# Performance work log

Hardware: AMD Instinct MI355X
Metric: run time of the kernel (lower is better)

Reference implementation:

```python
import jax, jax.numpy as jnp
import numpy as np

B, NMAX, D, NUM = 1024, 128, 256, 4
EPS = 1e-8
NEG = -1e9


def segment_softmax(logits, seg):
    # torch_geometric-style softmax over ragged segments. logits: (T,)
    m = jax.ops.segment_max(logits, seg, num_segments=B)
    e = jnp.exp(logits - m[seg])
    s = jax.ops.segment_sum(e, seg, num_segments=B)
    return e / (s[seg] + 1e-16)


def to_dense(v, seg, pos):
    # scatter ragged rows into (B, NMAX, ...) dense batch
    return jnp.zeros((B, NMAX) + v.shape[1:], v.dtype).at[seg, pos].set(v)


def uot_badmm(x, q0d, maskf, a1, a2, a3, rho):
    # Bregman-ADMM solver for entropic unbalanced OT (f_method='badmm-e').
    # x: (B,N,D) cost (to be maximized); q0d, maskf: (B,N,1); a1,a2,a3,rho: (NUM,)
    log_p0 = jnp.full((B, 1, D), -jnp.log(float(D)), x.dtype)  # uniform dim prior
    log_q0 = jnp.log(q0d + EPS)                                # (B,N,1)
    log_t = log_q0 + log_p0                                    # T init = q0 p0^T
    log_s = log_t
    log_mu = log_p0
    log_eta = log_q0
    z = jnp.zeros_like(x)
    z1 = jnp.zeros_like(log_p0)
    z2 = jnp.zeros_like(log_q0)
    neg = (1.0 - maskf) * NEG  # exclude padded rows from N-axis softmax
    for k in range(NUM):
        r, b1, b2, b3 = rho[k], a1[k], a2[k], a3[k]
        # T-update: rows (over D) sum to eta
        y = (x - z + r * log_s) / (b2 + r)
        log_t = log_eta + jax.nn.log_softmax(y, axis=2)
        # S-update: columns (over N) sum to mu, masked
        y = (z + r * log_t) / (b1 + r) + neg
        log_s = log_mu + jax.nn.log_softmax(y, axis=1)
        # unbalanced marginal updates (KL to priors, weight a3)
        log_mu = (b3 * log_p0 - z1 + r * jax.nn.logsumexp(log_s, axis=1, keepdims=True)) / (b3 + r)
        log_eta = (b3 * log_q0 - z2 + r * jax.nn.logsumexp(log_t, axis=2, keepdims=True)) / (b3 + r)
        # dual ascent
        t = jnp.exp(log_t) * maskf
        s = jnp.exp(log_s) * maskf
        z = z + r * (t - s)
        z1 = z1 + r * (jnp.exp(log_mu) - jnp.sum(s, axis=1, keepdims=True))
        z2 = z2 + r * (jnp.exp(log_eta) - jnp.sum(t, axis=2, keepdims=True)) * maskf
    return jnp.exp(log_t) * maskf


def setup_inputs() -> dict:
    rng = np.random.default_rng(0)
    lengths = rng.integers(NMAX // 2, NMAX + 1, size=B)
    lengths[0] = NMAX  # ensure max size present
    batch = jnp.asarray(np.repeat(np.arange(B), lengths), dtype=jnp.int32)
    total = int(lengths.sum())
    ks = jax.random.split(jax.random.key(0), 8)
    x = jax.random.normal(ks[0], (total, D), jnp.float32)
    W1 = jax.random.normal(ks[1], (2 * D, D), jnp.float32) / np.float32(np.sqrt(D))
    W2 = jax.random.normal(ks[2], (1, 2 * D), jnp.float32) / np.float32(np.sqrt(2 * D))
    rho = 0.1 * jax.random.normal(ks[3], (NUM,), jnp.float32)
    a1 = 0.1 * jax.random.normal(ks[4], (NUM,), jnp.float32)
    a2 = 0.1 * jax.random.normal(ks[5], (NUM,), jnp.float32)
    a3 = 0.1 * jax.random.normal(ks[6], (NUM,), jnp.float32)
    return {"x": x, "batch": batch, "W1": W1, "W2": W2, "rho": rho, "a1": a1, "a2": a2, "a3": a3}


def reference(x, batch, W1, W2, rho, a1, a2, a3):
    # attention-based sample prior q0 (q0 != 'fixed' branch)
    h = jnp.tanh(x @ W1.T)          # (T, 2D)
    logits = (h @ W2.T)[:, 0]       # (T,)
    q0 = segment_softmax(logits, batch)[:, None]  # (T, 1)
    # ragged -> dense batch (to_dense_batch)
    counts = jax.ops.segment_sum(jnp.ones_like(batch), batch, num_segments=B)
    starts = jnp.cumsum(counts) - counts
    pos = jnp.arange(batch.shape[0]) - starts[batch]
    xd = to_dense(x, batch, pos)    # (B, NMAX, D)
    q0d = to_dense(q0, batch, pos)  # (B, NMAX, 1)
    mask = to_dense(jnp.ones((batch.shape[0], 1), x.dtype), batch, pos)  # (B, NMAX, 1)
    trans = uot_badmm(xd, q0d, mask,
                      jax.nn.softplus(a1), jax.nn.softplus(a2),
                      jax.nn.softplus(a3), jax.nn.softplus(rho))
    frot = D * xd * trans * mask    # (B, NMAX, D)
    return jnp.sum(frot, axis=1)    # (B, D)
```

## Files before the change

### kernel.cpp

```cpp
#include <hip/hip_runtime.h>
#include <math.h>

#define BB   1024
#define DD   256
#define LOGD 5.5451774444795624753f
#define RST  260

typedef __attribute__((ext_vector_type(8))) short short8;
typedef __attribute__((ext_vector_type(4))) float f32x4;

__device__ __forceinline__ float wave_sum(float v){
  #pragma unroll
  for (int off=32; off>0; off>>=1) v += __shfl_xor(v, off, 64);
  return v;
}
__device__ __forceinline__ float wave_max(float v){
  #pragma unroll
  for (int off=32; off>0; off>>=1) v = fmaxf(v, __shfl_xor(v, off, 64));
  return v;
}
__device__ __forceinline__ float grp_sum(float v){
  v += __shfl_xor(v, 1, 64);
  v += __shfl_xor(v, 2, 64);
  v += __shfl_xor(v, 4, 64);
  v += __shfl_xor(v, 8, 64);
  return v;
}
__device__ __forceinline__ float fast_tanh(float x){
  return 1.0f - 2.0f/(__expf(2.0f*x)+1.0f);
}
__device__ __forceinline__ unsigned short f2bf(float f){
  unsigned int u = __float_as_uint(f);
  unsigned int r = u + 0x7FFFu + ((u >> 16) & 1u);
  return (unsigned short)(r >> 16);
}
__device__ __forceinline__ float decq(int q16){ return (float)q16 * (1.0f/512.0f); }
__device__ __forceinline__ int   zenc(float z){
  float t = fmaf(z, 4096.0f, 12582912.0f);
  return __float_as_int(t) - 0x4B400000;
}
__device__ __forceinline__ float zdec(int q){ return (float)q * (1.0f/4096.0f); }
__device__ __forceinline__ int lo16(unsigned u){ return ((int)(u<<16))>>16; }
__device__ __forceinline__ int hi16(unsigned u){ return ((int)u)>>16; }
__device__ __forceinline__ unsigned pk2(int a, int b){
  return ((unsigned)a & 0xffffu) | ((unsigned)b << 16);
}
__device__ __forceinline__ unsigned pkadd_sat(unsigned a, unsigned b){
  unsigned d; asm("v_pk_add_i16 %0, %1, %2 clamp" : "=v"(d) : "v"(a), "v"(b)); return d;
}

__global__ void k_pre(const float* __restrict__ W1, unsigned short* __restrict__ w1b,
                      const int* __restrict__ batch, int T, int* __restrict__ starts,
                      const float* __restrict__ rho, const float* __restrict__ a1,
                      const float* __restrict__ a2, const float* __restrict__ a3,
                      float* __restrict__ P)
{
  const int blk = blockIdx.x, tid = threadIdx.x;
  if (blk < 64){
    const int t = blk*256 + tid;
    #pragma unroll
    for (int i=0;i<2;i++){
      const int idx = (t*2 + i)*4;
      const float4 v = *(const float4*)(W1 + idx);
      *(ushort4*)(w1b + idx) = make_ushort4(f2bf(v.x), f2bf(v.y), f2bf(v.z), f2bf(v.w));
    }
  } else if (blk < 69){
    const int b = (blk-64)*256 + tid;
    if (b <= BB){
      int lo = 0, hi = T;
      while (lo < hi){ int mid = (lo+hi)>>1; if (batch[mid] < b) lo = mid+1; else hi = mid; }
      starts[b] = lo;
    }
  } else {
    if (tid == 0){
      float lm = -LOGD, z1 = 0.f;
      for (int k=0;k<4;k++){
        float r  = log1pf(expf(rho[k]));
        float b1 = log1pf(expf(a1[k]));
        float b2 = log1pf(expf(a2[k]));
        float b3 = log1pf(expf(a3[k]));
        P[k]    = r;
        P[4+k]  = 1.f/(b1+r);
        P[8+k]  = 1.f/(b2+r);
        P[12+k] = lm;
        P[16+k] = b3;
        P[20+k] = 1.f/(b3+r);
        float lmn = (b3*(-LOGD) - z1 + r*lm)/(b3+r);
        z1 += r*(expf(lmn)-expf(lm));
        lm = lmn;
      }
    }
  }
}

#define LPW 72
#define XST 264
__global__ __launch_bounds__(512) __attribute__((amdgpu_waves_per_eu(2, 4)))
void k_mlp(
    const float* __restrict__ x, const unsigned short* __restrict__ w1b,
    const float* __restrict__ W2, float* __restrict__ logits, int T)
{
  __shared__ unsigned short Xs[128*XST];
  __shared__ unsigned short Ws[128*LPW];
  __shared__ float lred[128];
  const int bx = blockIdx.x;
  const int tid = threadIdx.x;
  if (tid < 128) lred[tid] = 0.f;

  const int l = tid & 63;
  const int w = tid >> 6;
  const int wm = w >> 2;
  const int wn = w & 3;
  const int lr = l & 15, quad = l >> 4;
  const int wrow = tid >> 3;
  const int wseg = tid & 7;

  {
    const int r = tid >> 2;
    const int s = tid & 3;
    const int grow = bx*128 + r;
    #pragma unroll 4
    for (int i=0;i<16;i++){
      float4 v = make_float4(0.f,0.f,0.f,0.f);
      if (grow < T) v = *(const float4*)(x + (size_t)grow*DD + s*64 + i*4);
      *(ushort4*)&Xs[r*XST + s*64 + i*4] =
          make_ushort4(f2bf(v.x), f2bf(v.y), f2bf(v.z), f2bf(v.w));
    }
  }

  for (int by=0; by<4; by++){
    f32x4 acc[4][2];
    #pragma unroll
    for (int mi=0;mi<4;mi++)
      #pragma unroll
      for (int ni=0;ni<2;ni++) acc[mi][ni] = (f32x4){0.f,0.f,0.f,0.f};

    for (int kt=0; kt<4; kt++){
      #pragma unroll
      for (int h=0; h<2; h++){
        const int r = h*64 + wrow;
        *(short8*)&Ws[r*LPW + wseg*8] =
            *(const short8*)(w1b + (size_t)(by*128 + r)*DD + kt*64 + wseg*8);
      }
      __syncthreads();
      #pragma unroll
      for (int ks=0; ks<2; ks++){
        short8 afr[4], bfr[2];
        #pragma unroll
        for (int mi=0;mi<4;mi++)
          afr[mi] = *(const short8*)&Xs[(wm*64 + mi*16 + lr)*XST + kt*64 + ks*32 + quad*8];
        #pragma unroll
        for (int ni=0;ni<2;ni++)
          bfr[ni] = *(const short8*)&Ws[(wn*32 + ni*16 + lr)*LPW + ks*32 + quad*8];
        #pragma unroll
        for (int mi=0;mi<4;mi++)
          #pragma unroll
          for (int ni=0;ni<2;ni++)
            acc[mi][ni] = __builtin_amdgcn_mfma_f32_16x16x32_bf16(afr[mi], bfr[ni], acc[mi][ni], 0, 0, 0);
      }
      __syncthreads();
    }

    float w2v[2];
    #pragma unroll
    for (int ni=0;ni<2;ni++) w2v[ni] = W2[by*128 + wn*32 + ni*16 + lr];
    #pragma unroll
    for (int mi=0;mi<4;mi++){
      float p[4];
      #pragma unroll
      for (int v=0; v<4; v++){
        p[v] = fast_tanh(acc[mi][0][v])*w2v[0] + fast_tanh(acc[mi][1][v])*w2v[1];
        #pragma unroll
        for (int off=1; off<16; off<<=1) p[v] += __shfl_xor(p[v], off, 64);
      }
      if (lr == 0){
        #pragma unroll
        for (int v=0; v<4; v++)
          atomicAdd(&lred[wm*64 + mi*16 + quad*4 + v], p[v]);
      }
    }
  }
  __syncthreads();
  if (tid < 128){
    const int grow = bx*128 + tid;
    if (grow < T) logits[grow] = lred[tid];
  }
}

__global__ __launch_bounds__(512) __attribute__((amdgpu_waves_per_eu(4, 6)))
void k_solver(
    const float* __restrict__ x, const float* __restrict__ logits,
    const int* __restrict__ starts, const float* __restrict__ P,
    float* __restrict__ out)
{
  __shared__ __align__(16) float red[32*RST];
  __shared__ __align__(16) float colv[DD];
  const int b = blockIdx.x;
  const int start = starts[b];
  const int len = starts[b+1] - start;
  const int tid = threadIdx.x;
  const int w = tid >> 6, l = tid & 63;
  const int sub = l >> 4;
  const int c0  = l & 15;
  const int n0 = w*16;
  int nv = len - n0; nv = nv < 0 ? 0 : (nv > 16 ? 16 : nv);

  const float r0=P[0], r1=P[1], r2=P[2], r3=P[3];
  const float i10=P[4], i11=P[5], i12=P[6];
  const float i20=P[8], i21=P[9], i22=P[10], i23=P[11];
  const float mu0=P[12], mu1=P[13], mu2=P[14];
  const float b30=P[16], b31=P[17], b32=P[18];
  const float e30=P[20], e31=P[21], e32=P[22];

  const float* lg = logits + start;
  float v0 = (l      < len) ? lg[l]    : -3.0e38f;
  float v1 = (l+64   < len) ? lg[l+64] : -3.0e38f;
  float sm = wave_max(fmaxf(v0,v1));
  float se0 = (l    < len) ? __expf(v0-sm) : 0.f;
  float se1 = (l+64 < len) ? __expf(v1-sm) : 0.f;
  float ssum0 = wave_sum(se0+se1);
  const float sinv = 1.f/(ssum0 + 1e-16f);
  const float esel = (n0 < 64) ? se0 : se1;

  float slqg[4], etag[4], z2g[4];
  uint2 ap[4][4];
  uint2 zp[4][4];
  #pragma unroll
  for (int g=0; g<4; g++){
    const int row = n0 + 4*g + sub;
    const float ev = __shfl(esel, row & 63, 64);
    const float lq = __logf(ev*sinv + 1e-8f);
    slqg[g] = lq; etag[g] = lq; z2g[g] = 0.f;
    #pragma unroll
    for (int q=0;q<4;q++){ zp[g][q].x = 0u; zp[g][q].y = 0u; }
  }

  const float* xbase = x + (size_t)(start + n0 + sub)*DD + 4*c0;

  {
    float sp[16];
    #pragma unroll
    for (int j=0;j<16;j++) sp[j]=0.f;
    #pragma unroll
    for (int g=0; g<4; g++){
      if (4*g + sub < nv){
        const float* xp = xbase + (size_t)(4*g)*DD;
        const float a0 = slqg[g] - LOGD;
        float ss = 0.f;
        #pragma unroll
        for (int q=0;q<4;q++){
          const float4 xv = *(const float4*)(xp + 64*q);
          const float xvv[4] = {xv.x, xv.y, xv.z, xv.w};
          int ny[4];
          #pragma unroll
          for (int j=0;j<4;j++){
            const float y = (xvv[j] + r0*a0) * i20;
            ss += __expf(y);
            ny[j] = __float2int_rn(y*512.f);
          }
          ap[g][q].x = pk2(ny[0],ny[1]);
          ap[g][q].y = pk2(ny[2],ny[3]);
        }
        ss = grp_sum(ss);
        const float off = etag[g] - __logf(ss);
        const int offi = __float2int_rn(fmaxf(off, -56.f)*512.f);
        const unsigned offpk = pk2(offi, offi);
        #pragma unroll
        for (int q=0;q<4;q++){
          ap[g][q].x = pkadd_sat(ap[g][q].x, offpk);
          ap[g][q].y = pkadd_sat(ap[g][q].y, offpk);
          sp[4*q+0] += __expf((r0*decq(lo16(ap[g][q].x))) * i10);
          sp[4*q+1] += __expf((r0*decq(hi16(ap[g][q].x))) * i10);
          sp[4*q+2] += __expf((r0*decq(lo16(ap[g][q].y))) * i10);
          sp[4*q+3] += __expf((r0*decq(hi16(ap[g][q].y))) * i10);
        }
        const float en = (b30*slqg[g] - z2g[g] + r0*etag[g]) * e30;
        z2g[g] += r0*(__expf(en) - __expf(etag[g]));
        etag[g] = en;
      }
    }
    #pragma unroll
    for (int q=0;q<4;q++)
      *(float4*)&red[(4*w+sub)*RST + 64*q + 4*c0] =
          make_float4(sp[4*q], sp[4*q+1], sp[4*q+2], sp[4*q+3]);
  }
  __syncthreads();
  if (tid < DD){
    float s = 0.f;
    #pragma unroll
    for (int i=0;i<32;i++) s += red[i*RST + tid];
    colv[tid] = __logf(s);
  }
  __syncthreads();

  #pragma unroll
  for (int k=1;k<3;k++){
    const float rkm = (k==1)? r0 : r1;
    const float ib1m= (k==1)? i10 : i11;
    const float mum = (k==1)? mu0 : mu1;
    const float rk  = (k==1)? r1 : r2;
    const float ib1k= (k==1)? i11 : i12;
    const float ib2k= (k==1)? i21 : i22;
    const float b3k = (k==1)? b31 : b32;
    const float e3k = (k==1)? e31 : e32;
    float sp[16];
    #pragma unroll
    for (int j=0;j<16;j++) sp[j]=0.f;
    #pragma unroll
    for (int g=0; g<4; g++){
      if (4*g + sub < nv){
        const float* xp = xbase + (size_t)(4*g)*DD;
        float ss = 0.f;
        #pragma unroll
        for (int q=0;q<4;q++){
          const float4 lscq = *(const float4*)&colv[64*q + 4*c0];
          const float4 xv   = *(const float4*)(xp + 64*q);
          const float xvv[4]  = {xv.x, xv.y, xv.z, xv.w};
          const float lscv[4] = {lscq.x, lscq.y, lscq.z, lscq.w};
          const int aq[4] = {lo16(ap[g][q].x), hi16(ap[g][q].x),
                             lo16(ap[g][q].y), hi16(ap[g][q].y)};
          const int zq[4] = {lo16(zp[g][q].x), hi16(zp[g][q].x),
                             lo16(zp[g][q].y), hi16(zp[g][q].y)};
          int ny[4], nz[4];
          #pragma unroll
          for (int j=0;j<4;j++){
            const float lt = decq(aq[j]);
            float zf = zdec(zq[j]);
            const float ys  = (zf + rkm*lt) * ib1m;
            const float lsn = mum + ys - lscv[j];
            zf += rkm*(__expf(lt) - __expf(lsn));
            nz[j] = zenc(zf);
            const float y = (xvv[j] - zdec(nz[j]) + rk*lsn) * ib2k;
            ss += __expf(y);
            ny[j] = __float2int_rn(y*512.f);
          }
          ap[g][q].x = pk2(ny[0],ny[1]);
          ap[g][q].y = pk2(ny[2],ny[3]);
          zp[g][q].x = pk2(nz[0],nz[1]);
          zp[g][q].y = pk2(nz[2],nz[3]);
        }
        ss = grp_sum(ss);
        const float off = etag[g] - __logf(ss);
        const int offi = __float2int_rn(fmaxf(off, -56.f)*512.f);
        const unsigned offpk = pk2(offi, offi);
        #pragma unroll
        for (int q=0;q<4;q++){
          ap[g][q].x = pkadd_sat(ap[g][q].x, offpk);
          ap[g][q].y = pkadd_sat(ap[g][q].y, offpk);
          sp[4*q+0] += __expf((zdec(lo16(zp[g][q].x)) + rk*decq(lo16(ap[g][q].x))) * ib1k);
          sp[4*q+1] += __expf((zdec(hi16(zp[g][q].x)) + rk*decq(hi16(ap[g][q].x))) * ib1k);
          sp[4*q+2] += __expf((zdec(lo16(zp[g][q].y)) + rk*decq(lo16(ap[g][q].y))) * ib1k);
          sp[4*q+3] += __expf((zdec(hi16(zp[g][q].y)) + rk*decq(hi16(ap[g][q].y))) * ib1k);
        }
        const float en = (b3k*slqg[g] - z2g[g] + rk*etag[g]) * e3k;
        z2g[g] += rk*(__expf(en) - __expf(etag[g]));
        etag[g] = en;
      }
    }
    #pragma unroll
    for (int q=0;q<4;q++)
      *(float4*)&red[(4*w+sub)*RST + 64*q + 4*c0] =
          make_float4(sp[4*q], sp[4*q+1], sp[4*q+2], sp[4*q+3]);
    __syncthreads();
    if (tid < DD){
      float s = 0.f;
      #pragma unroll
      for (int i=0;i<32;i++) s += red[i*RST + tid];
      colv[tid] = __logf(s);
    }
    __syncthreads();
  }

  {
    float op[16];
    #pragma unroll
    for (int j=0;j<16;j++) op[j]=0.f;
    #pragma unroll
    for (int g=0; g<4; g++){
      if (4*g + sub < nv){
        const float* xp = xbase + (size_t)(4*g)*DD;
        float ey[16];
        float ss = 0.f;
        #pragma unroll
        for (int q=0;q<4;q++){
          const float4 lscq = *(const float4*)&colv[64*q + 4*c0];
          const float4 xv   = *(const float4*)(xp + 64*q);
          const float xvv[4]  = {xv.x, xv.y, xv.z, xv.w};
          const float lscv[4] = {lscq.x, lscq.y, lscq.z, lscq.w};
          const int aq[4] = {lo16(ap[g][q].x), hi16(ap[g][q].x),
                             lo16(ap[g][q].y), hi16(ap[g][q].y)};
          const int zq[4] = {lo16(zp[g][q].x), hi16(zp[g][q].x),
                             lo16(zp[g][q].y), hi16(zp[g][q].y)};
          #pragma unroll
          for (int j=0;j<4;j++){
            const float lt = decq(aq[j]);
            float zf = zdec(zq[j]);
            const float ys  = (zf + r2*lt) * i12;
            const float lsn = mu2 + ys - lscv[j];
            zf += r2*(__expf(lt) - __expf(lsn));
            const float y = (xvv[j] - zf + r3*lsn) * i23;
            const float e = __expf(y);
            ey[4*q+j] = e;
            ss += e;
          }
        }
        ss = grp_sum(ss);
        const float rs = __expf(etag[g]) / ss;
        #pragma unroll
        for (int q=0;q<4;q++){
          const float4 xv = *(const float4*)(xp + 64*q);
          op[4*q+0] += xv.x * ey[4*q+0] * rs;
          op[4*q+1] += xv.y * ey[4*q+1] * rs;
          op[4*q+2] += xv.z * ey[4*q+2] * rs;
          op[4*q+3] += xv.w * ey[4*q+3] * rs;
        }
      }
    }
    #pragma unroll
    for (int q=0;q<4;q++)
      *(float4*)&red[(4*w+sub)*RST + 64*q + 4*c0] =
          make_float4(op[4*q], op[4*q+1], op[4*q+2], op[4*q+3]);
    __syncthreads();
    if (tid < DD){
      float s = 0.f;
      #pragma unroll
      for (int i=0;i<32;i++) s += red[i*RST + tid];
      out[(size_t)b*DD + tid] = 256.0f * s;
    }
  }
}

extern "C" void kernel_launch(void* const* d_in, const int* in_sizes, int n_in,
                              void* d_out, int out_size, void* d_ws, size_t ws_size,
                              hipStream_t stream) {
  const float* x    = (const float*)d_in[0];
  const int*   batch= (const int*)d_in[1];
  const float* W1   = (const float*)d_in[2];
  const float* W2   = (const float*)d_in[3];
  const float* rho  = (const float*)d_in[4];
  const float* a1   = (const float*)d_in[5];
  const float* a2   = (const float*)d_in[6];
  const float* a3   = (const float*)d_in[7];
  float* out = (float*)d_out;
  const int T = in_sizes[1];

  float* logits = (float*)d_ws;
  int*   starts = (int*)(logits + T);
  float* P      = (float*)(starts + 1028);
  unsigned short* w1b = (unsigned short*)(P + 32);

  k_pre<<<70, 256, 0, stream>>>(W1, w1b, batch, T, starts, rho, a1, a2, a3, P);
  k_mlp<<<(T+127)/128, 512, 0, stream>>>(x, w1b, W2, logits, T);
  k_solver<<<BB, 512, 0, stream>>>(x, logits, starts, P, out);
}
```

Measured before the change: 383.6 us.

## Double-buffer W1 tiles in MLP kernel and double its threads per block

The MLP logits kernel now runs with 1024 threads, so each wave computes a 32x32 output sub-tile instead of 64x32. The W1 tile in shared memory is double-buffered, and the by/kt loops are flattened into one 16-step loop. The next tile is loaded while the current one is consumed, which cuts the barriers per step from two to one. In exchange each block uses more LDS and more threads, which can lower occupancy, and the per-wave MFMA work between barriers is smaller.

```diff
diff --git a/kernel.cpp b/kernel.cpp
--- a/kernel.cpp
+++ b/kernel.cpp
@@ -95,13 +95,13 @@
 
 #define LPW 72
 #define XST 264
-__global__ __launch_bounds__(512) __attribute__((amdgpu_waves_per_eu(2, 4)))
+__global__ __launch_bounds__(1024) __attribute__((amdgpu_waves_per_eu(2, 4)))
 void k_mlp(
     const float* __restrict__ x, const unsigned short* __restrict__ w1b,
     const float* __restrict__ W2, float* __restrict__ logits, int T)
 {
   __shared__ unsigned short Xs[128*XST];
-  __shared__ unsigned short Ws[128*LPW];
+  __shared__ unsigned short Ws[2][128*LPW];
   __shared__ float lred[128];
   const int bx = blockIdx.x;
   const int tid = threadIdx.x;
@@ -112,75 +112,79 @@
   const int wm = w >> 2;
   const int wn = w & 3;
   const int lr = l & 15, quad = l >> 4;
-  const int wrow = tid >> 3;
-  const int wseg = tid & 7;
+  const int sr = tid >> 3;
+  const int sc = tid & 7;
 
   {
-    const int r = tid >> 2;
-    const int s = tid & 3;
-    const int grow = bx*128 + r;
-    #pragma unroll 4
-    for (int i=0;i<16;i++){
+    const int grow = bx*128 + sr;
+    #pragma unroll
+    for (int i=0;i<8;i++){
       float4 v = make_float4(0.f,0.f,0.f,0.f);
-      if (grow < T) v = *(const float4*)(x + (size_t)grow*DD + s*64 + i*4);
-      *(ushort4*)&Xs[r*XST + s*64 + i*4] =
+      if (grow < T) v = *(const float4*)(x + (size_t)grow*DD + sc*32 + i*4);
+      *(ushort4*)&Xs[sr*XST + sc*32 + i*4] =
           make_ushort4(f2bf(v.x), f2bf(v.y), f2bf(v.z), f2bf(v.w));
     }
   }
-
-  for (int by=0; by<4; by++){
-    f32x4 acc[4][2];
-    #pragma unroll
-    for (int mi=0;mi<4;mi++)
-      #pragma unroll
-      for (int ni=0;ni<2;ni++) acc[mi][ni] = (f32x4){0.f,0.f,0.f,0.f};
-
-    for (int kt=0; kt<4; kt++){
-      #pragma unroll
-      for (int h=0; h<2; h++){
-        const int r = h*64 + wrow;
-        *(short8*)&Ws[r*LPW + wseg*8] =
-            *(const short8*)(w1b + (size_t)(by*128 + r)*DD + kt*64 + wseg*8);
+  *(short8*)&Ws[0][sr*LPW + sc*8] =
+      *(const short8*)(w1b + (size_t)sr*DD + sc*8);
+  __syncthreads();
+
+  f32x4 acc[2][2];
+  #pragma unroll
+  for (int mi=0;mi<2;mi++)
+    #pragma unroll
+    for (int ni=0;ni<2;ni++) acc[mi][ni] = (f32x4){0.f,0.f,0.f,0.f};
+
+  for (int t=0; t<16; ++t){
+    const int by = t >> 2, kt = t & 3;
+    if (t < 15){
+      const int nby = (t+1) >> 2, nkt = (t+1) & 3;
+      *(short8*)&Ws[(t+1)&1][sr*LPW + sc*8] =
+          *(const short8*)(w1b + (size_t)(nby*128 + sr)*DD + nkt*64 + sc*8);
+    }
+    const unsigned short* wbuf = Ws[t&1];
+    #pragma unroll
+    for (int ks=0; ks<2; ks++){
+      short8 afr[2], bfr[2];
+      #pragma unroll
+      for (int mi=0;mi<2;mi++)
+        afr[mi] = *(const short8*)&Xs[(wm*32 + mi*16 + lr)*XST + kt*64 + ks*32 + quad*8];
+      #pragma unroll
+      for (int ni=0;ni<2;ni++)
+        bfr[ni] = *(const short8*)&wbuf[(wn*32 + ni*16 + lr)*LPW + ks*32 + quad*8];
+      #pragma unroll
+      for (int mi=0;mi<2;mi++)
+        #pragma unroll
+        for (int ni=0;ni<2;ni++)
+          acc[mi][ni] = __builtin_amdgcn_mfma_f32_16x16x32_bf16(afr[mi], bfr[ni], acc[mi][ni], 0, 0, 0);
+    }
+    if (kt == 3){
+      float w2v[2];
+      #pragma unroll
+      for (int ni=0;ni<2;ni++) w2v[ni] = W2[by*128 + wn*32 + ni*16 + lr];
+      #pragma unroll
+      for (int mi=0;mi<2;mi++){
+        float p[4];
+        #pragma unroll
+        for (int v=0; v<4; v++){
+          p[v] = fast_tanh(acc[mi][0][v])*w2v[0] + fast_tanh(acc[mi][1][v])*w2v[1];
+          #pragma unroll
+          for (int off=1; off<16; off<<=1) p[v] += __shfl_xor(p[v], off, 64);
+        }
+        if (lr == 0){
+          #pragma unroll
+          for (int v=0; v<4; v++)
+            atomicAdd(&lred[wm*32 + mi*16 + quad*4 + v], p[v]);
+        }
       }
-      __syncthreads();
-      #pragma unroll
-      for (int ks=0; ks<2; ks++){
-        short8 afr[4], bfr[2];
-        #pragma unroll
-        for (int mi=0;mi<4;mi++)
-          afr[mi] = *(const short8*)&Xs[(wm*64 + mi*16 + lr)*XST + kt*64 + ks*32 + quad*8];
-        #pragma unroll
-        for (int ni=0;ni<2;ni++)
-          bfr[ni] = *(const short8*)&Ws[(wn*32 + ni*16 + lr)*LPW + ks*32 + quad*8];
-        #pragma unroll
-        for (int mi=0;mi<4;mi++)
-          #pragma unroll
-          for (int ni=0;ni<2;ni++)
-            acc[mi][ni] = __builtin_amdgcn_mfma_f32_16x16x32_bf16(afr[mi], bfr[ni], acc[mi][ni], 0, 0, 0);
-      }
-      __syncthreads();
-    }
-
-    float w2v[2];
-    #pragma unroll
-    for (int ni=0;ni<2;ni++) w2v[ni] = W2[by*128 + wn*32 + ni*16 + lr];
-    #pragma unroll
-    for (int mi=0;mi<4;mi++){
-      float p[4];
-      #pragma unroll
-      for (int v=0; v<4; v++){
-        p[v] = fast_tanh(acc[mi][0][v])*w2v[0] + fast_tanh(acc[mi][1][v])*w2v[1];
-        #pragma unroll
-        for (int off=1; off<16; off<<=1) p[v] += __shfl_xor(p[v], off, 64);
-      }
-      if (lr == 0){
-        #pragma unroll
-        for (int v=0; v<4; v++)
-          atomicAdd(&lred[wm*64 + mi*16 + quad*4 + v], p[v]);
-      }
-    }
-  }
-  __syncthreads();
+      #pragma unroll
+      for (int mi=0;mi<2;mi++)
+        #pragma unroll
+        for (int ni=0;ni<2;ni++) acc[mi][ni] = (f32x4){0.f,0.f,0.f,0.f};
+    }
+    __syncthreads();
+  }
+
   if (tid < 128){
     const int grow = bx*128 + tid;
     if (grow < T) logits[grow] = lred[tid];
@@ -450,6 +454,6 @@
   unsigned short* w1b = (unsigned short*)(P + 32);
 
   k_pre<<<70, 256, 0, stream>>>(W1, w1b, batch, T, starts, rho, a1, a2, a3, P);
-  k_mlp<<<(T+127)/128, 512, 0, stream>>>(x, w1b, W2, logits, T);
+  k_mlp<<<(T+127)/128, 1024, 0, stream>>>(x, w1b, W2, logits, T);
   k_solver<<<BB, 512, 0, stream>>>(x, logits, starts, P, out);
 }
```

New measurement: 389.1 us. No clear change (+1.4%).

## Fuse attention MLP into solver kernel, computing per-segment logits in LDS

Applied to the files above, without the earlier changes.

Removes the separate k_mlp launch and computes each segment's attention logits inside the solver block, using MFMA with x read directly from global memory and W1 bf16 fragments loaded straight from global. Logits now live in shared memory instead of a global round trip. This drops one kernel launch and the logits write/read. In exchange, the solver kernel's occupancy hint drops from (4,6) to (2,4) waves per EU, register pressure grows, and W1 is re-read by every block without LDS staging. Padded rows are recomputed with a clamped row index.

```diff
diff --git a/kernel.cpp b/kernel.cpp
--- a/kernel.cpp
+++ b/kernel.cpp
@@ -33,6 +33,12 @@
   unsigned int u = __float_as_uint(f);
   unsigned int r = u + 0x7FFFu + ((u >> 16) & 1u);
   return (unsigned short)(r >> 16);
+}
+__device__ __forceinline__ short8 pack_bf16_8(float4 a, float4 b){
+  union { ushort4 h[2]; short8 s; } u;
+  u.h[0] = make_ushort4(f2bf(a.x), f2bf(a.y), f2bf(a.z), f2bf(a.w));
+  u.h[1] = make_ushort4(f2bf(b.x), f2bf(b.y), f2bf(b.z), f2bf(b.w));
+  return u.s;
 }
 __device__ __forceinline__ float decq(int q16){ return (float)q16 * (1.0f/512.0f); }
 __device__ __forceinline__ int   zenc(float z){
@@ -93,108 +99,16 @@
   }
 }
 
-#define LPW 72
-#define XST 264
 __global__ __launch_bounds__(512) __attribute__((amdgpu_waves_per_eu(2, 4)))
-void k_mlp(
+void k_solver(
     const float* __restrict__ x, const unsigned short* __restrict__ w1b,
-    const float* __restrict__ W2, float* __restrict__ logits, int T)
-{
-  __shared__ unsigned short Xs[128*XST];
-  __shared__ unsigned short Ws[128*LPW];
-  __shared__ float lred[128];
-  const int bx = blockIdx.x;
-  const int tid = threadIdx.x;
-  if (tid < 128) lred[tid] = 0.f;
-
-  const int l = tid & 63;
-  const int w = tid >> 6;
-  const int wm = w >> 2;
-  const int wn = w & 3;
-  const int lr = l & 15, quad = l >> 4;
-  const int wrow = tid >> 3;
-  const int wseg = tid & 7;
-
-  {
-    const int r = tid >> 2;
-    const int s = tid & 3;
-    const int grow = bx*128 + r;
-    #pragma unroll 4
-    for (int i=0;i<16;i++){
-      float4 v = make_float4(0.f,0.f,0.f,0.f);
-      if (grow < T) v = *(const float4*)(x + (size_t)grow*DD + s*64 + i*4);
-      *(ushort4*)&Xs[r*XST + s*64 + i*4] =
-          make_ushort4(f2bf(v.x), f2bf(v.y), f2bf(v.z), f2bf(v.w));
-    }
-  }
-
-  for (int by=0; by<4; by++){
-    f32x4 acc[4][2];
-    #pragma unroll
-    for (int mi=0;mi<4;mi++)
-      #pragma unroll
-      for (int ni=0;ni<2;ni++) acc[mi][ni] = (f32x4){0.f,0.f,0.f,0.f};
-
-    for (int kt=0; kt<4; kt++){
-      #pragma unroll
-      for (int h=0; h<2; h++){
-        const int r = h*64 + wrow;
-        *(short8*)&Ws[r*LPW + wseg*8] =
-            *(const short8*)(w1b + (size_t)(by*128 + r)*DD + kt*64 + wseg*8);
-      }
-      __syncthreads();
-      #pragma unroll
-      for (int ks=0; ks<2; ks++){
-        short8 afr[4], bfr[2];
-        #pragma unroll
-        for (int mi=0;mi<4;mi++)
-          afr[mi] = *(const short8*)&Xs[(wm*64 + mi*16 + lr)*XST + kt*64 + ks*32 + quad*8];
-        #pragma unroll
-        for (int ni=0;ni<2;ni++)
-          bfr[ni] = *(const short8*)&Ws[(wn*32 + ni*16 + lr)*LPW + ks*32 + quad*8];
-        #pragma unroll
-        for (int mi=0;mi<4;mi++)
-          #pragma unroll
-          for (int ni=0;ni<2;ni++)
-            acc[mi][ni] = __builtin_amdgcn_mfma_f32_16x16x32_bf16(afr[mi], bfr[ni], acc[mi][ni], 0, 0, 0);
-      }
-      __syncthreads();
-    }
-
-    float w2v[2];
-    #pragma unroll
-    for (int ni=0;ni<2;ni++) w2v[ni] = W2[by*128 + wn*32 + ni*16 + lr];
-    #pragma unroll
-    for (int mi=0;mi<4;mi++){
-      float p[4];
-      #pragma unroll
-      for (int v=0; v<4; v++){
-        p[v] = fast_tanh(acc[mi][0][v])*w2v[0] + fast_tanh(acc[mi][1][v])*w2v[1];
-        #pragma unroll
-        for (int off=1; off<16; off<<=1) p[v] += __shfl_xor(p[v], off, 64);
-      }
-      if (lr == 0){
-        #pragma unroll
-        for (int v=0; v<4; v++)
-          atomicAdd(&lred[wm*64 + mi*16 + quad*4 + v], p[v]);
-      }
-    }
-  }
-  __syncthreads();
-  if (tid < 128){
-    const int grow = bx*128 + tid;
-    if (grow < T) logits[grow] = lred[tid];
-  }
-}
-
-__global__ __launch_bounds__(512) __attribute__((amdgpu_waves_per_eu(4, 6)))
-void k_solver(
-    const float* __restrict__ x, const float* __restrict__ logits,
+    const float* __restrict__ W2,
     const int* __restrict__ starts, const float* __restrict__ P,
     float* __restrict__ out)
 {
   __shared__ __align__(16) float red[32*RST];
   __shared__ __align__(16) float colv[DD];
+  __shared__ float lred[128];
   const int b = blockIdx.x;
   const int start = starts[b];
   const int len = starts[b+1] - start;
@@ -202,8 +116,67 @@
   const int w = tid >> 6, l = tid & 63;
   const int sub = l >> 4;
   const int c0  = l & 15;
+  const int lr  = l & 15, quad = l >> 4;
   const int n0 = w*16;
   int nv = len - n0; nv = nv < 0 ? 0 : (nv > 16 ? 16 : nv);
+
+  if (tid < 128) lred[tid] = 0.f;
+  __syncthreads();
+
+  {
+    const int hb = w*64;
+    float w2v[4];
+    #pragma unroll
+    for (int nt=0;nt<4;nt++) w2v[nt] = W2[hb + nt*16 + lr];
+
+    for (int mc=0; mc<2; ++mc){
+      f32x4 acc[4][4];
+      #pragma unroll
+      for (int mt=0;mt<4;mt++)
+        #pragma unroll
+        for (int nt=0;nt<4;nt++) acc[mt][nt] = (f32x4){0.f,0.f,0.f,0.f};
+
+      const float* xr[4];
+      #pragma unroll
+      for (int mt=0;mt<4;mt++){
+        int r = mc*64 + mt*16 + lr;
+        r = (r < len) ? r : (len-1);
+        xr[mt] = x + (size_t)(start + r)*DD + quad*8;
+      }
+      #pragma unroll
+      for (int ks=0; ks<8; ++ks){
+        short8 bfr[4];
+        #pragma unroll
+        for (int nt=0;nt<4;nt++)
+          bfr[nt] = *(const short8*)(w1b + (size_t)(hb + nt*16 + lr)*DD + ks*32 + quad*8);
+        #pragma unroll
+        for (int mt=0;mt<4;mt++){
+          const float* p = xr[mt] + ks*32;
+          const short8 afr = pack_bf16_8(*(const float4*)p, *(const float4*)(p+4));
+          #pragma unroll
+          for (int nt=0;nt<4;nt++)
+            acc[mt][nt] = __builtin_amdgcn_mfma_f32_16x16x32_bf16(afr, bfr[nt], acc[mt][nt], 0, 0, 0);
+        }
+      }
+      #pragma unroll
+      for (int mt=0;mt<4;mt++){
+        float p[4];
+        #pragma unroll
+        for (int v=0; v<4; v++){
+          p[v] = fast_tanh(acc[mt][0][v])*w2v[0] + fast_tanh(acc[mt][1][v])*w2v[1]
+               + fast_tanh(acc[mt][2][v])*w2v[2] + fast_tanh(acc[mt][3][v])*w2v[3];
+          #pragma unroll
+          for (int off=1; off<16; off<<=1) p[v] += __shfl_xor(p[v], off, 64);
+        }
+        if (lr == 0){
+          #pragma unroll
+          for (int v=0; v<4; v++)
+            atomicAdd(&lred[mc*64 + mt*16 + quad*4 + v], p[v]);
+        }
+      }
+    }
+  }
+  __syncthreads();
 
   const float r0=P[0], r1=P[1], r2=P[2], r3=P[3];
   const float i10=P[4], i11=P[5], i12=P[6];
@@ -212,9 +185,8 @@
   const float b30=P[16], b31=P[17], b32=P[18];
   const float e30=P[20], e31=P[21], e32=P[22];
 
-  const float* lg = logits + start;
-  float v0 = (l      < len) ? lg[l]    : -3.0e38f;
-  float v1 = (l+64   < len) ? lg[l+64] : -3.0e38f;
+  float v0 = (l      < len) ? lred[l]    : -3.0e38f;
+  float v1 = (l+64   < len) ? lred[l+64] : -3.0e38f;
   float sm = wave_max(fmaxf(v0,v1));
   float se0 = (l    < len) ? __expf(v0-sm) : 0.f;
   float se1 = (l+64 < len) ? __expf(v1-sm) : 0.f;
@@ -450,6 +422,5 @@
   unsigned short* w1b = (unsigned short*)(P + 32);
 
   k_pre<<<70, 256, 0, stream>>>(W1, w1b, batch, T, starts, rho, a1, a2, a3, P);
-  k_mlp<<<(T+127)/128, 512, 0, stream>>>(x, w1b, W2, logits, T);
-  k_solver<<<BB, 512, 0, stream>>>(x, logits, starts, P, out);
-}
+  k_solver<<<BB, 512, 0, stream>>>(x, w1b, W2, starts, P, out);
+}
```

After: 446.1 us. +16.3%, slower.
